# Kernel tuning notes

Hardware: AMD Instinct MI355X
Metric: run time of the kernel (lower is better)

Reference implementation:

```python
import jax, jax.numpy as jnp
import numpy as np

B1, B2, D = 10000, 10000, 128
ORDER = 4


def _cdist(a, b):
    # Stable L2 distance matrix: (B1,B2)
    a2 = jnp.sum(a * a, axis=1)[:, None]
    b2 = jnp.sum(b * b, axis=1)[None, :]
    d2 = a2 + b2 - 2.0 * (a @ b.T)
    return jnp.sqrt(jnp.clip(d2, 0.0))


def setup_inputs() -> dict:
    key = jax.random.key(0)
    k1, k2, k3 = jax.random.split(key, 3)
    desc1 = jax.random.normal(k1, (B1, D), dtype=jnp.float32)
    desc2 = jax.random.normal(k2, (B2, D), dtype=jnp.float32)
    # Steerer generator (D,D); scaled so repeated application stays bounded.
    generator = jax.random.normal(k3, (D, D), dtype=jnp.float32) / np.sqrt(D)
    return {"desc1": desc1, "desc2": desc2, "generator": generator, "steerer_order": ORDER}


def reference(desc1, desc2, generator, steerer_order):
    # steer_mode='local': distance between a pair is the min over all
    # steered versions of desc1 (DiscreteSteerer applies F.linear(x, G),
    # i.e. x @ G.T, repeatedly).
    dm = _cdist(desc1, desc2)
    d = desc1
    for _ in range(steerer_order - 1):
        d = d @ generator.T
        dm = jnp.minimum(dm, _cdist(d, desc2))
    # match_mode='nn': nearest neighbor in desc2 for each row of desc1.
    match_dists = jnp.min(dm, axis=1)
    idxs_in_2 = jnp.argmin(dm, axis=1)
    idxs_in_1 = jnp.arange(dm.shape[0], dtype=jnp.int64 if jax.config.jax_enable_x64 else jnp.int32)
    matches_idxs = jnp.stack([idxs_in_1, idxs_in_2.astype(idxs_in_1.dtype)], axis=1)
    return match_dists[:, None], matches_idxs
```

## Files before the change

### kernel.cpp

```cpp
#include <hip/hip_runtime.h>
#include <hip/hip_fp16.h>
#include <math.h>

#define NB1 10000
#define NB2 10000
#define DD  128
#define NV  4
#define B1P 10048
#define B1R (B1P * NV)
#define NB2P 10112
#define NB2G 320
#define NJT 79
#define MB  256
#define BN  128
#define NCHUNK 6
#define SROWS 16
#define SCALE 64.0f

typedef _Float16 f16x8 __attribute__((ext_vector_type(8)));
typedef __attribute__((ext_vector_type(16))) float f32x16;

__device__ __forceinline__ void gload_lds16(const void* g, void* l) {
    __builtin_amdgcn_global_load_lds(
        (const __attribute__((address_space(1))) void*)g,
        (__attribute__((address_space(3))) void*)l, 16, 0, 0);
}
__device__ __forceinline__ f32x16 mfma16(f16x8 a, f16x8 b, f32x16 c) {
    return __builtin_amdgcn_mfma_f32_32x32x16_f16(a, b, c, 0, 0, 0);
}
__device__ __forceinline__ void enc(float x, unsigned short* hb, unsigned short* lb) {
    float xs = SCALE * x;
    __half hh = __float2half_rn(xs);
    __half hl = __float2half_rn(xs - __half2float(hh));
    *hb = __half_as_ushort(hh);
    *lb = __half_as_ushort(hl);
}
__device__ __forceinline__ size_t cmap(int row, int col) {
    return ((size_t)(row >> 5) * 16 + (col >> 4)) * 512
         + (size_t)((row & 31) + (((col >> 3) & 1) << 5)) * 8 + (col & 7);
}


__global__ __launch_bounds__(128) void prep1s_kernel(
    const float* __restrict__ desc1, const float* __restrict__ G,
    unsigned short* __restrict__ A2c, float* __restrict__ n1) {
    __shared__ float GTl[128 * 129];
    __shared__ float src[SROWS][DD];
    __shared__ float p2[SROWS][2];
    const int t = threadIdx.x;
    const int i0 = blockIdx.x * SROWS;
    for (int f = 0; f < DD; ++f)
        GTl[t * 129 + f] = G[(size_t)f * DD + t];
    for (int r = 0; r < SROWS; ++r)
        src[r][t] = (i0 + r < NB1) ? desc1[(size_t)(i0 + r) * DD + t] : 0.f;
    __syncthreads();
    for (int k = 0; k < NV; ++k) {
        if (k > 0) {
            float out[SROWS];
#pragma unroll
            for (int r = 0; r < SROWS; ++r) out[r] = 0.f;
            for (int c = 0; c < DD; ++c) {
                float g = GTl[c * 129 + t];
#pragma unroll
                for (int r = 0; r < SROWS; ++r) out[r] = fmaf(src[r][c], g, out[r]);
            }
            __syncthreads();
#pragma unroll
            for (int r = 0; r < SROWS; ++r) src[r][t] = out[r];
            __syncthreads();
        }
        for (int r = 0; r < SROWS; ++r) {
            float x = src[r][t];
            unsigned short hb, lb;
            enc(x, &hb, &lb);
            int ar = (i0 + r) * NV + k;
            A2c[cmap(ar, t)] = hb;
            A2c[cmap(ar, 128 + t)] = lb;
            float s = x * x;
            for (int off = 32; off; off >>= 1) s += __shfl_down(s, off);
            if ((t & 63) == 0) p2[r][t >> 6] = s;
        }
        __syncthreads();
        if (t < SROWS) n1[(i0 + t) * NV + k] = p2[t][0] + p2[t][1];
        __syncthreads();
    }
}

__global__ void prep2_kernel(const float* __restrict__ desc2,
                             unsigned short* __restrict__ B2c, float* __restrict__ n2) {
    int j = blockIdx.x;
    int t = threadIdx.x;
    float x = (j < NB2) ? desc2[j * DD + t] : 0.f;
    unsigned short hb, lb;
    enc(x, &hb, &lb);
    B2c[cmap(j, t)] = hb;
    B2c[cmap(j, 128 + t)] = lb;
    float s = x * x;
    for (int off = 32; off; off >>= 1) s += __shfl_down(s, off);
    __shared__ float p[2];
    if ((t & 63) == 0) p[t >> 6] = s;
    __syncthreads();
    if (t == 0) n2[j] = (j < NB2) ? (p[0] + p[1]) : 1e30f;
}


#define STAGE1(BSEL, J0V, C16B, HALF)                                             \
    {                                                                             \
        int k16h_ = w >> 2, nf_ = w & 3;                                          \
        size_t gc_ = (size_t)(((J0V) >> 5) + nf_) * 16 + (C16B) + (HALF) * 2 + k16h_; \
        gload_lds16((const char*)B2c + gc_ * 1024 + l * 16,                       \
                    LDSB + (BSEL) * 8192 + w * 1024 + l * 16);                    \
    }

#define COMP2(BSEL, HALF, AK0, AK1)                                               \
    {                                                                             \
        _Pragma("unroll")                                                         \
        for (int kh_ = 0; kh_ < 2; ++kh_) {                                       \
            f16x8 b0_ = *(const f16x8*)(LDSB + (BSEL) * 8192 + (kh_ * 4 + wn * 2 + 0) * 1024 + l * 16); \
            f16x8 b1_ = *(const f16x8*)(LDSB + (BSEL) * 8192 + (kh_ * 4 + wn * 2 + 1) * 1024 + l * 16); \
            acc[0][0] = mfma16(Areg[0][AK0][(HALF) * 2 + kh_], b0_, acc[0][0]);   \
            acc[0][1] = mfma16(Areg[0][AK0][(HALF) * 2 + kh_], b1_, acc[0][1]);   \
            acc[1][0] = mfma16(Areg[1][AK0][(HALF) * 2 + kh_], b0_, acc[1][0]);   \
            acc[1][1] = mfma16(Areg[1][AK0][(HALF) * 2 + kh_], b1_, acc[1][1]);   \
            acc[0][0] = mfma16(Areg[0][AK1][(HALF) * 2 + kh_], b0_, acc[0][0]);   \
            acc[0][1] = mfma16(Areg[0][AK1][(HALF) * 2 + kh_], b1_, acc[0][1]);   \
            acc[1][0] = mfma16(Areg[1][AK1][(HALF) * 2 + kh_], b0_, acc[1][0]);   \
            acc[1][1] = mfma16(Areg[1][AK1][(HALF) * 2 + kh_], b1_, acc[1][1]);   \
        }                                                                         \
    }

#define COMP1(BSEL, HALF, AK0)                                                    \
    {                                                                             \
        _Pragma("unroll")                                                         \
        for (int kh_ = 0; kh_ < 2; ++kh_) {                                       \
            f16x8 b0_ = *(const f16x8*)(LDSB + (BSEL) * 8192 + (kh_ * 4 + wn * 2 + 0) * 1024 + l * 16); \
            f16x8 b1_ = *(const f16x8*)(LDSB + (BSEL) * 8192 + (kh_ * 4 + wn * 2 + 1) * 1024 + l * 16); \
            acc[0][0] = mfma16(Areg[0][AK0][(HALF) * 2 + kh_], b0_, acc[0][0]);   \
            acc[0][1] = mfma16(Areg[0][AK0][(HALF) * 2 + kh_], b1_, acc[0][1]);   \
            acc[1][0] = mfma16(Areg[1][AK0][(HALF) * 2 + kh_], b0_, acc[1][0]);   \
            acc[1][1] = mfma16(Areg[1][AK0][(HALF) * 2 + kh_], b1_, acc[1][1]);   \
        }                                                                         \
    }

#define PH(VM, BS, J0S, C16S, HS, CMP)                           \
    asm volatile("s_waitcnt vmcnt(" VM ")" ::: "memory");        \
    __builtin_amdgcn_s_barrier();                                \
    __builtin_amdgcn_sched_barrier(0);                           \
    STAGE1(BS, J0S, C16S, HS);                                   \
    CMP

__global__ __launch_bounds__(512, 2) void match_kernel(
    const unsigned short* __restrict__ A2c, const unsigned short* __restrict__ B2c,
    const float* __restrict__ n1, const float* __restrict__ n2,
    float* __restrict__ pb, int* __restrict__ pj) {
    __shared__ __align__(16) char LDSB[4 * 8192];
    __shared__ float LDSn1[256];
    const int t = threadIdx.x;
    const int l = t & 63, w = t >> 6;
    const int wm = w >> 1, wn = w & 1;
    const int c5 = l & 31, h = l >> 5;
    const int bi = blockIdx.x, ch = blockIdx.y;
    const int R0 = bi * MB;

    f16x8 Areg[2][4][4];
#pragma unroll
    for (int a = 0; a < 2; ++a)
#pragma unroll
        for (int aks = 0; aks < 4; ++aks)
#pragma unroll
            for (int k16 = 0; k16 < 4; ++k16) {
                size_t g = (size_t)(bi * 8 + wm * 2 + a);
                Areg[a][aks][k16] = *(const f16x8*)(
                    (const char*)A2c + (g * 16 + aks * 4 + k16) * 1024 + l * 16);
            }
    { int idx = t & 255; LDSn1[idx] = n1[R0 + idx]; }

    const int jt0 = (ch * NJT) / NCHUNK;
    const int jt1 = ((ch + 1) * NJT) / NCHUNK;

    STAGE1(0, jt0 * BN, 0, 0);
    STAGE1(1, jt0 * BN, 0, 1);
    STAGE1(2, jt0 * BN, 4, 0);
    asm volatile("s_waitcnt lgkmcnt(0)" ::: "memory");

    float best[2][4];
    int bj[2][4];
#pragma unroll
    for (int a = 0; a < 2; ++a)
#pragma unroll
        for (int rq = 0; rq < 4; ++rq) { best[a][rq] = 3.4e38f; bj[a][rq] = 0; }

    for (int jt = jt0; jt < jt1; ++jt) {
        const int j0 = jt * BN;
        float nn0 = n2[j0 + wn * 64 + c5];
        float nn1 = n2[j0 + wn * 64 + 32 + c5];
        f32x16 acc[2][2];
#pragma unroll
        for (int a = 0; a < 2; ++a)
#pragma unroll
            for (int b = 0; b < 2; ++b)
#pragma unroll
                for (int e = 0; e < 16; ++e) acc[a][b][e] = 0.f;

        PH("4", 3, j0, 4, 1,       COMP2(0, 0, 0, 2));
        PH("4", 0, j0, 8, 0,       COMP2(1, 1, 0, 2));
        PH("4", 1, j0, 8, 1,       COMP2(2, 0, 1, 3));
        PH("2", 2, j0, 12, 0,      COMP2(3, 1, 1, 3));
        PH("2", 3, j0, 12, 1,      COMP1(0, 0, 0));
        PH("2", 0, j0 + BN, 0, 0,  COMP1(1, 1, 0));
        PH("2", 1, j0 + BN, 0, 1,  COMP1(2, 0, 1));
        PH("2", 2, j0 + BN, 4, 0,  COMP1(3, 1, 1));

#pragma unroll
        for (int a = 0; a < 2; ++a)
#pragma unroll
            for (int b = 0; b < 2; ++b) {
                float nn = b ? nn1 : nn0;
                int j = j0 + wn * 64 + b * 32 + c5;
#pragma unroll
                for (int rq = 0; rq < 4; ++rq) {
                    float4 n1v = *(const float4*)&LDSn1[wm * 64 + a * 32 + 8 * rq + 4 * h];
                    float e0 = fmaf(-0.00048828125f, acc[a][b][4 * rq + 0], n1v.x);
                    float e1 = fmaf(-0.00048828125f, acc[a][b][4 * rq + 1], n1v.y);
                    float e2 = fmaf(-0.00048828125f, acc[a][b][4 * rq + 2], n1v.z);
                    float e3 = fmaf(-0.00048828125f, acc[a][b][4 * rq + 3], n1v.w);
                    float d = fminf(fminf(e0, e1), fminf(e2, e3)) + nn;
                    if (d < best[a][rq]) { best[a][rq] = d; bj[a][rq] = j; }
                }
            }
    }

#pragma unroll
    for (int off = 1; off < 32; off <<= 1) {
#pragma unroll
        for (int a = 0; a < 2; ++a)
#pragma unroll
            for (int rq = 0; rq < 4; ++rq) {
                float ov = __shfl_xor(best[a][rq], off);
                int oj = __shfl_xor(bj[a][rq], off);
                if (ov < best[a][rq] || (ov == best[a][rq] && oj < bj[a][rq])) {
                    best[a][rq] = ov; bj[a][rq] = oj;
                }
            }
    }
    if (c5 == 0) {
        int slot = ch * 2 + wn;
#pragma unroll
        for (int a = 0; a < 2; ++a)
#pragma unroll
            for (int rq = 0; rq < 4; ++rq) {
                int i = bi * 64 + wm * 16 + a * 8 + 2 * rq + h;
                pb[slot * B1P + i] = best[a][rq];
                pj[slot * B1P + i] = bj[a][rq];
            }
    }
}

__global__ void final_kernel(const float* __restrict__ pb, const int* __restrict__ pj,
                             float* __restrict__ out) {
    int i = blockIdx.x * 256 + threadIdx.x;
    if (i < NB1) {
        float bv = 3.4e38f;
        int bj = 0;
#pragma unroll
        for (int s = 0; s < 2 * NCHUNK; ++s) {
            float v = pb[s * B1P + i];
            int j = pj[s * B1P + i];
            if (v < bv || (v == bv && j < bj)) { bv = v; bj = j; }
        }
        out[i] = sqrtf(fmaxf(bv, 0.f));
        out[NB1 + 2 * i] = (float)i;
        out[NB1 + 2 * i + 1] = (float)bj;
    }
}


extern "C" void kernel_launch(void* const* d_in, const int* in_sizes, int n_in,
                              void* d_out, int out_size, void* d_ws, size_t ws_size,
                              hipStream_t stream) {
    const float* desc1 = (const float*)d_in[0];
    const float* desc2 = (const float*)d_in[1];
    const float* G     = (const float*)d_in[2];

    unsigned short* A2c = (unsigned short*)d_ws;
    unsigned short* B2c = A2c + (size_t)(B1R / 32) * 16 * 512;
    float* n1 = (float*)(B2c + (size_t)NB2G * 16 * 512);
    float* n2 = n1 + B1R;
    float* pb = n2 + NB2P;
    int*   pj = (int*)(pb + 2 * NCHUNK * B1P);
    float* out = (float*)d_out;

    hipLaunchKernelGGL(prep1s_kernel, dim3(B1P / SROWS), dim3(128), 0, stream,
                       desc1, G, A2c, n1);
    hipLaunchKernelGGL(prep2_kernel, dim3(NB2P), dim3(128), 0, stream, desc2, B2c, n2);
    hipLaunchKernelGGL(match_kernel, dim3(B1R / MB, NCHUNK), dim3(512), 0, stream,
                       A2c, B2c, n1, n2, pb, pj);
    hipLaunchKernelGGL(final_kernel, dim3((NB1 + 255) / 256), dim3(256), 0, stream,
                       pb, pj, out);
}
```

Before: 455.2 us.

## Restructure prep kernels with LDS-staged coalesced writes and halve match row tile

The prep kernels now build each 32-row fragment block in shared memory and write it out with coalesced 16-byte stores, instead of scattered 2-byte writes through cmap. A separate transpose kernel produces GT in global memory so prep1 no longer loads a 64KB G transpose into LDS per block. The match kernel halves the row tile to 128 (one 32-row fragment per wave), stages whole 4-k16 B slices per phase into larger LDS buffers with 4 phases instead of 8, and raises wave priority around the MFMA blocks. NCHUNK drops to 3 so the grid stays the same size. Fewer A registers may raise occupancy, but each B tile fetched is now reused across fewer A rows.

```diff
diff --git a/kernel.cpp b/kernel.cpp
--- a/kernel.cpp
+++ b/kernel.cpp
@@ -11,10 +11,9 @@
 #define NB2P 10112
 #define NB2G 320
 #define NJT 79
-#define MB  256
+#define MB  128
 #define BN  128
-#define NCHUNK 6
-#define SROWS 16
+#define NCHUNK 3
 #define SCALE 64.0f
 
 typedef _Float16 f16x8 __attribute__((ext_vector_type(8)));
@@ -35,126 +34,159 @@
     *hb = __half_as_ushort(hh);
     *lb = __half_as_ushort(hl);
 }
-__device__ __forceinline__ size_t cmap(int row, int col) {
-    return ((size_t)(row >> 5) * 16 + (col >> 4)) * 512
-         + (size_t)((row & 31) + (((col >> 3) & 1) << 5)) * 8 + (col & 7);
-}
-
-
-__global__ __launch_bounds__(128) void prep1s_kernel(
-    const float* __restrict__ desc1, const float* __restrict__ G,
+
+
+__global__ void gt_kernel(const float* __restrict__ G, float* __restrict__ GT) {
+    int idx = blockIdx.x * 256 + threadIdx.x;
+    if (idx < DD * DD) {
+        int c = idx / DD, f = idx % DD;
+        GT[idx] = G[f * DD + c];
+    }
+}
+
+__global__ __launch_bounds__(128) void prep1_kernel(
+    const float* __restrict__ desc1, const float* __restrict__ GT,
     unsigned short* __restrict__ A2c, float* __restrict__ n1) {
-    __shared__ float GTl[128 * 129];
-    __shared__ float src[SROWS][DD];
-    __shared__ float p2[SROWS][2];
+    __shared__ float src[8][DD];
+    __shared__ __align__(16) unsigned short cbuf[8192];
+    __shared__ float p2[8][2];
     const int t = threadIdx.x;
-    const int i0 = blockIdx.x * SROWS;
-    for (int f = 0; f < DD; ++f)
-        GTl[t * 129 + f] = G[(size_t)f * DD + t];
-    for (int r = 0; r < SROWS; ++r)
+    const int i0 = blockIdx.x * 8;
+    for (int r = 0; r < 8; ++r)
         src[r][t] = (i0 + r < NB1) ? desc1[(size_t)(i0 + r) * DD + t] : 0.f;
     __syncthreads();
     for (int k = 0; k < NV; ++k) {
-        if (k > 0) {
-            float out[SROWS];
-#pragma unroll
-            for (int r = 0; r < SROWS; ++r) out[r] = 0.f;
+        float out[8];
+        if (k == 0) {
+#pragma unroll
+            for (int r = 0; r < 8; ++r) out[r] = src[r][t];
+        } else {
+#pragma unroll
+            for (int r = 0; r < 8; ++r) out[r] = 0.f;
             for (int c = 0; c < DD; ++c) {
-                float g = GTl[c * 129 + t];
-#pragma unroll
-                for (int r = 0; r < SROWS; ++r) out[r] = fmaf(src[r][c], g, out[r]);
+                float g = GT[c * DD + t];
+#pragma unroll
+                for (int r = 0; r < 8; ++r) out[r] = fmaf(src[r][c], g, out[r]);
             }
             __syncthreads();
 #pragma unroll
-            for (int r = 0; r < SROWS; ++r) src[r][t] = out[r];
+            for (int r = 0; r < 8; ++r) src[r][t] = out[r];
             __syncthreads();
         }
-        for (int r = 0; r < SROWS; ++r) {
-            float x = src[r][t];
+        const int c16h = t >> 4, half = (t >> 3) & 1, el = t & 7;
+        for (int r = 0; r < 8; ++r) {
             unsigned short hb, lb;
-            enc(x, &hb, &lb);
-            int ar = (i0 + r) * NV + k;
-            A2c[cmap(ar, t)] = hb;
-            A2c[cmap(ar, 128 + t)] = lb;
-            float s = x * x;
+            enc(out[r], &hb, &lb);
+            int row32 = r * 4 + k;
+            cbuf[c16h * 512 + (row32 + half * 32) * 8 + el] = hb;
+            cbuf[(8 + c16h) * 512 + (row32 + half * 32) * 8 + el] = lb;
+            float s = out[r] * out[r];
             for (int off = 32; off; off >>= 1) s += __shfl_down(s, off);
             if ((t & 63) == 0) p2[r][t >> 6] = s;
         }
         __syncthreads();
-        if (t < SROWS) n1[(i0 + t) * NV + k] = p2[t][0] + p2[t][1];
+        if (t < 8) n1[(size_t)(i0 + t) * NV + k] = p2[t][0] + p2[t][1];
         __syncthreads();
     }
-}
-
-__global__ void prep2_kernel(const float* __restrict__ desc2,
-                             unsigned short* __restrict__ B2c, float* __restrict__ n2) {
-    int j = blockIdx.x;
-    int t = threadIdx.x;
-    float x = (j < NB2) ? desc2[j * DD + t] : 0.f;
-    unsigned short hb, lb;
-    enc(x, &hb, &lb);
-    B2c[cmap(j, t)] = hb;
-    B2c[cmap(j, 128 + t)] = lb;
-    float s = x * x;
-    for (int off = 32; off; off >>= 1) s += __shfl_down(s, off);
-    __shared__ float p[2];
-    if ((t & 63) == 0) p[t >> 6] = s;
+    const int wv = t >> 6, l = t & 63;
+#pragma unroll
+    for (int q = 0; q < 8; ++q) {
+        int chunk = wv * 8 + q;
+        int4 v = *(const int4*)((const char*)cbuf + chunk * 1024 + l * 16);
+        *(int4*)((char*)A2c + ((size_t)blockIdx.x * 16 + chunk) * 1024 + l * 16) = v;
+    }
+}
+
+__global__ __launch_bounds__(256) void prep2_kernel(
+    const float* __restrict__ desc2, unsigned short* __restrict__ B2c,
+    float* __restrict__ n2) {
+    __shared__ float srcf[32 * DD];
+    __shared__ __align__(16) unsigned short cbuf[8192];
+    const int t = threadIdx.x;
+    const int j0 = blockIdx.x * 32;
+    for (int ii = 0; ii < 16; ++ii) {
+        int idx = t + 256 * ii;
+        int row = idx >> 7, col = idx & 127;
+        srcf[idx] = (j0 + row < NB2) ? desc2[(size_t)(j0 + row) * DD + col] : 0.f;
+    }
     __syncthreads();
-    if (t == 0) n2[j] = (j < NB2) ? (p[0] + p[1]) : 1e30f;
-}
-
-
-#define STAGE1(BSEL, J0V, C16B, HALF)                                             \
-    {                                                                             \
-        int k16h_ = w >> 2, nf_ = w & 3;                                          \
-        size_t gc_ = (size_t)(((J0V) >> 5) + nf_) * 16 + (C16B) + (HALF) * 2 + k16h_; \
-        gload_lds16((const char*)B2c + gc_ * 1024 + l * 16,                       \
-                    LDSB + (BSEL) * 8192 + w * 1024 + l * 16);                    \
-    }
-
-#define COMP2(BSEL, HALF, AK0, AK1)                                               \
+    const int r = t >> 3, cg = t & 7;
+    float s = 0.f;
+#pragma unroll
+    for (int e = 0; e < 16; ++e) {
+        int c = cg * 16 + e;
+        float x = srcf[r * DD + c];
+        unsigned short hb, lb;
+        enc(x, &hb, &lb);
+        int lane = r + ((e >> 3) & 1) * 32;
+        cbuf[cg * 512 + lane * 8 + (e & 7)] = hb;
+        cbuf[(8 + cg) * 512 + lane * 8 + (e & 7)] = lb;
+        s += x * x;
+    }
+    s += __shfl_xor(s, 1); s += __shfl_xor(s, 2); s += __shfl_xor(s, 4);
+    if ((t & 7) == 0) n2[j0 + r] = (j0 + r < NB2) ? s : 1e30f;
+    __syncthreads();
+    const int wv = t >> 6, l = t & 63;
+#pragma unroll
+    for (int q = 0; q < 4; ++q) {
+        int chunk = wv * 4 + q;
+        int4 v = *(const int4*)((const char*)cbuf + chunk * 1024 + l * 16);
+        *(int4*)((char*)B2c + ((size_t)blockIdx.x * 16 + chunk) * 1024 + l * 16) = v;
+    }
+}
+
+
+#define STAGE(BUF, J0V, C16B)                                                     \
     {                                                                             \
         _Pragma("unroll")                                                         \
-        for (int kh_ = 0; kh_ < 2; ++kh_) {                                       \
-            f16x8 b0_ = *(const f16x8*)(LDSB + (BSEL) * 8192 + (kh_ * 4 + wn * 2 + 0) * 1024 + l * 16); \
-            f16x8 b1_ = *(const f16x8*)(LDSB + (BSEL) * 8192 + (kh_ * 4 + wn * 2 + 1) * 1024 + l * 16); \
-            acc[0][0] = mfma16(Areg[0][AK0][(HALF) * 2 + kh_], b0_, acc[0][0]);   \
-            acc[0][1] = mfma16(Areg[0][AK0][(HALF) * 2 + kh_], b1_, acc[0][1]);   \
-            acc[1][0] = mfma16(Areg[1][AK0][(HALF) * 2 + kh_], b0_, acc[1][0]);   \
-            acc[1][1] = mfma16(Areg[1][AK0][(HALF) * 2 + kh_], b1_, acc[1][1]);   \
-            acc[0][0] = mfma16(Areg[0][AK1][(HALF) * 2 + kh_], b0_, acc[0][0]);   \
-            acc[0][1] = mfma16(Areg[0][AK1][(HALF) * 2 + kh_], b1_, acc[0][1]);   \
-            acc[1][0] = mfma16(Areg[1][AK1][(HALF) * 2 + kh_], b0_, acc[1][0]);   \
-            acc[1][1] = mfma16(Areg[1][AK1][(HALF) * 2 + kh_], b1_, acc[1][1]);   \
+        for (int c_ = 0; c_ < 2; ++c_) {                                          \
+            int chunk_ = w * 2 + c_;                                              \
+            int nf_ = chunk_ >> 2, c16_ = chunk_ & 3;                             \
+            size_t gc_ = (size_t)(((J0V) >> 5) + nf_) * 16 + (C16B) + c16_;       \
+            gload_lds16((const char*)B2c + gc_ * 1024 + l * 16,                   \
+                        LDSB + (BUF) * 16384 + chunk_ * 1024 + l * 16);           \
         }                                                                         \
     }
 
-#define COMP1(BSEL, HALF, AK0)                                                    \
+#define COMP2(BUF, AKA, AKB)                                                      \
     {                                                                             \
         _Pragma("unroll")                                                         \
-        for (int kh_ = 0; kh_ < 2; ++kh_) {                                       \
-            f16x8 b0_ = *(const f16x8*)(LDSB + (BSEL) * 8192 + (kh_ * 4 + wn * 2 + 0) * 1024 + l * 16); \
-            f16x8 b1_ = *(const f16x8*)(LDSB + (BSEL) * 8192 + (kh_ * 4 + wn * 2 + 1) * 1024 + l * 16); \
-            acc[0][0] = mfma16(Areg[0][AK0][(HALF) * 2 + kh_], b0_, acc[0][0]);   \
-            acc[0][1] = mfma16(Areg[0][AK0][(HALF) * 2 + kh_], b1_, acc[0][1]);   \
-            acc[1][0] = mfma16(Areg[1][AK0][(HALF) * 2 + kh_], b0_, acc[1][0]);   \
-            acc[1][1] = mfma16(Areg[1][AK0][(HALF) * 2 + kh_], b1_, acc[1][1]);   \
+        for (int k16_ = 0; k16_ < 4; ++k16_) {                                    \
+            f16x8 b0_ = *(const f16x8*)(LDSB + (BUF) * 16384 + ((wn * 2 + 0) * 4 + k16_) * 1024 + l * 16); \
+            f16x8 b1_ = *(const f16x8*)(LDSB + (BUF) * 16384 + ((wn * 2 + 1) * 4 + k16_) * 1024 + l * 16); \
+            acc[0] = mfma16(Areg[AKA][k16_], b0_, acc[0]);                        \
+            acc[1] = mfma16(Areg[AKA][k16_], b1_, acc[1]);                        \
+            acc[0] = mfma16(Areg[AKB][k16_], b0_, acc[0]);                        \
+            acc[1] = mfma16(Areg[AKB][k16_], b1_, acc[1]);                        \
         }                                                                         \
     }
 
-#define PH(VM, BS, J0S, C16S, HS, CMP)                           \
+#define COMP1(BUF, AKA)                                                           \
+    {                                                                             \
+        _Pragma("unroll")                                                         \
+        for (int k16_ = 0; k16_ < 4; ++k16_) {                                    \
+            f16x8 b0_ = *(const f16x8*)(LDSB + (BUF) * 16384 + ((wn * 2 + 0) * 4 + k16_) * 1024 + l * 16); \
+            f16x8 b1_ = *(const f16x8*)(LDSB + (BUF) * 16384 + ((wn * 2 + 1) * 4 + k16_) * 1024 + l * 16); \
+            acc[0] = mfma16(Areg[AKA][k16_], b0_, acc[0]);                        \
+            acc[1] = mfma16(Areg[AKA][k16_], b1_, acc[1]);                        \
+        }                                                                         \
+    }
+
+#define PH(VM, STG, CMP)                                         \
     asm volatile("s_waitcnt vmcnt(" VM ")" ::: "memory");        \
     __builtin_amdgcn_s_barrier();                                \
     __builtin_amdgcn_sched_barrier(0);                           \
-    STAGE1(BS, J0S, C16S, HS);                                   \
-    CMP
+    STG;                                                         \
+    __builtin_amdgcn_s_setprio(1);                               \
+    CMP;                                                         \
+    __builtin_amdgcn_s_setprio(0);
 
 __global__ __launch_bounds__(512, 2) void match_kernel(
     const unsigned short* __restrict__ A2c, const unsigned short* __restrict__ B2c,
     const float* __restrict__ n1, const float* __restrict__ n2,
     float* __restrict__ pb, int* __restrict__ pj) {
-    __shared__ __align__(16) char LDSB[4 * 8192];
-    __shared__ float LDSn1[256];
+    __shared__ __align__(16) char LDSB[4 * 16384];
+    __shared__ float LDSn1[128];
     const int t = threadIdx.x;
     const int l = t & 63, w = t >> 6;
     const int wm = w >> 1, wn = w & 1;
@@ -162,97 +194,81 @@
     const int bi = blockIdx.x, ch = blockIdx.y;
     const int R0 = bi * MB;
 
-    f16x8 Areg[2][4][4];
-#pragma unroll
-    for (int a = 0; a < 2; ++a)
-#pragma unroll
-        for (int aks = 0; aks < 4; ++aks)
-#pragma unroll
-            for (int k16 = 0; k16 < 4; ++k16) {
-                size_t g = (size_t)(bi * 8 + wm * 2 + a);
-                Areg[a][aks][k16] = *(const f16x8*)(
-                    (const char*)A2c + (g * 16 + aks * 4 + k16) * 1024 + l * 16);
-            }
-    { int idx = t & 255; LDSn1[idx] = n1[R0 + idx]; }
+    f16x8 Areg[4][4];
+#pragma unroll
+    for (int aks = 0; aks < 4; ++aks)
+#pragma unroll
+        for (int k16 = 0; k16 < 4; ++k16) {
+            size_t g = (size_t)(bi * 4 + wm);
+            Areg[aks][k16] = *(const f16x8*)(
+                (const char*)A2c + (g * 16 + aks * 4 + k16) * 1024 + l * 16);
+        }
+    if (t < 128) LDSn1[t] = n1[R0 + t];
 
     const int jt0 = (ch * NJT) / NCHUNK;
     const int jt1 = ((ch + 1) * NJT) / NCHUNK;
 
-    STAGE1(0, jt0 * BN, 0, 0);
-    STAGE1(1, jt0 * BN, 0, 1);
-    STAGE1(2, jt0 * BN, 4, 0);
+    STAGE(0, jt0 * BN, 0);
+    STAGE(1, jt0 * BN, 4);
+    STAGE(2, jt0 * BN, 8);
     asm volatile("s_waitcnt lgkmcnt(0)" ::: "memory");
 
-    float best[2][4];
-    int bj[2][4];
-#pragma unroll
-    for (int a = 0; a < 2; ++a)
-#pragma unroll
-        for (int rq = 0; rq < 4; ++rq) { best[a][rq] = 3.4e38f; bj[a][rq] = 0; }
+    float best[4];
+    int bj[4];
+#pragma unroll
+    for (int rq = 0; rq < 4; ++rq) { best[rq] = 3.4e38f; bj[rq] = 0; }
 
     for (int jt = jt0; jt < jt1; ++jt) {
         const int j0 = jt * BN;
         float nn0 = n2[j0 + wn * 64 + c5];
         float nn1 = n2[j0 + wn * 64 + 32 + c5];
-        f32x16 acc[2][2];
-#pragma unroll
-        for (int a = 0; a < 2; ++a)
-#pragma unroll
-            for (int b = 0; b < 2; ++b)
-#pragma unroll
-                for (int e = 0; e < 16; ++e) acc[a][b][e] = 0.f;
-
-        PH("4", 3, j0, 4, 1,       COMP2(0, 0, 0, 2));
-        PH("4", 0, j0, 8, 0,       COMP2(1, 1, 0, 2));
-        PH("4", 1, j0, 8, 1,       COMP2(2, 0, 1, 3));
-        PH("2", 2, j0, 12, 0,      COMP2(3, 1, 1, 3));
-        PH("2", 3, j0, 12, 1,      COMP1(0, 0, 0));
-        PH("2", 0, j0 + BN, 0, 0,  COMP1(1, 1, 0));
-        PH("2", 1, j0 + BN, 0, 1,  COMP1(2, 0, 1));
-        PH("2", 2, j0 + BN, 4, 0,  COMP1(3, 1, 1));
-
-#pragma unroll
-        for (int a = 0; a < 2; ++a)
-#pragma unroll
-            for (int b = 0; b < 2; ++b) {
-                float nn = b ? nn1 : nn0;
-                int j = j0 + wn * 64 + b * 32 + c5;
-#pragma unroll
-                for (int rq = 0; rq < 4; ++rq) {
-                    float4 n1v = *(const float4*)&LDSn1[wm * 64 + a * 32 + 8 * rq + 4 * h];
-                    float e0 = fmaf(-0.00048828125f, acc[a][b][4 * rq + 0], n1v.x);
-                    float e1 = fmaf(-0.00048828125f, acc[a][b][4 * rq + 1], n1v.y);
-                    float e2 = fmaf(-0.00048828125f, acc[a][b][4 * rq + 2], n1v.z);
-                    float e3 = fmaf(-0.00048828125f, acc[a][b][4 * rq + 3], n1v.w);
-                    float d = fminf(fminf(e0, e1), fminf(e2, e3)) + nn;
-                    if (d < best[a][rq]) { best[a][rq] = d; bj[a][rq] = j; }
-                }
+        f32x16 acc[2];
+#pragma unroll
+        for (int b = 0; b < 2; ++b)
+#pragma unroll
+            for (int e = 0; e < 16; ++e) acc[b][e] = 0.f;
+
+        PH("6", STAGE(3, j0, 12),      COMP2(0, 0, 2));
+        PH("6", STAGE(0, j0 + BN, 0),  COMP2(1, 1, 3));
+        PH("6", STAGE(1, j0 + BN, 4),  COMP1(2, 0));
+        PH("4", STAGE(2, j0 + BN, 8),  COMP1(3, 1));
+
+#pragma unroll
+        for (int b = 0; b < 2; ++b) {
+            float nn = b ? nn1 : nn0;
+            int j = j0 + wn * 64 + b * 32 + c5;
+#pragma unroll
+            for (int rq = 0; rq < 4; ++rq) {
+                float4 n1v = *(const float4*)&LDSn1[wm * 32 + 8 * rq + 4 * h];
+                float e0 = fmaf(-0.00048828125f, acc[b][4 * rq + 0], n1v.x);
+                float e1 = fmaf(-0.00048828125f, acc[b][4 * rq + 1], n1v.y);
+                float e2 = fmaf(-0.00048828125f, acc[b][4 * rq + 2], n1v.z);
+                float e3 = fmaf(-0.00048828125f, acc[b][4 * rq + 3], n1v.w);
+                float d = fminf(fminf(e0, e1), fminf(e2, e3)) + nn;
+                if (d < best[rq]) { best[rq] = d; bj[rq] = j; }
             }
+        }
     }
 
 #pragma unroll
     for (int off = 1; off < 32; off <<= 1) {
 #pragma unroll
-        for (int a = 0; a < 2; ++a)
-#pragma unroll
-            for (int rq = 0; rq < 4; ++rq) {
-                float ov = __shfl_xor(best[a][rq], off);
-                int oj = __shfl_xor(bj[a][rq], off);
-                if (ov < best[a][rq] || (ov == best[a][rq] && oj < bj[a][rq])) {
-                    best[a][rq] = ov; bj[a][rq] = oj;
-                }
+        for (int rq = 0; rq < 4; ++rq) {
+            float ov = __shfl_xor(best[rq], off);
+            int oj = __shfl_xor(bj[rq], off);
+            if (ov < best[rq] || (ov == best[rq] && oj < bj[rq])) {
+                best[rq] = ov; bj[rq] = oj;
             }
+        }
     }
     if (c5 == 0) {
         int slot = ch * 2 + wn;
 #pragma unroll
-        for (int a = 0; a < 2; ++a)
-#pragma unroll
-            for (int rq = 0; rq < 4; ++rq) {
-                int i = bi * 64 + wm * 16 + a * 8 + 2 * rq + h;
-                pb[slot * B1P + i] = best[a][rq];
-                pj[slot * B1P + i] = bj[a][rq];
-            }
+        for (int rq = 0; rq < 4; ++rq) {
+            int i = bi * 32 + wm * 8 + 2 * rq + h;
+            pb[slot * B1P + i] = best[rq];
+            pj[slot * B1P + i] = bj[rq];
+        }
     }
 }
 
@@ -283,16 +299,19 @@
     const float* G     = (const float*)d_in[2];
 
     unsigned short* A2c = (unsigned short*)d_ws;
-    unsigned short* B2c = A2c + (size_t)(B1R / 32) * 16 * 512;
-    float* n1 = (float*)(B2c + (size_t)NB2G * 16 * 512);
+    unsigned short* B2c = A2c + (size_t)(B1R / 32) * 8192;
+    float* GT = (float*)(B2c + (size_t)NB2G * 8192);
+    float* n1 = GT + DD * DD;
     float* n2 = n1 + B1R;
     float* pb = n2 + NB2P;
     int*   pj = (int*)(pb + 2 * NCHUNK * B1P);
     float* out = (float*)d_out;
 
-    hipLaunchKernelGGL(prep1s_kernel, dim3(B1P / SROWS), dim3(128), 0, stream,
-                       desc1, G, A2c, n1);
-    hipLaunchKernelGGL(prep2_kernel, dim3(NB2P), dim3(128), 0, stream, desc2, B2c, n2);
+    hipLaunchKernelGGL(gt_kernel, dim3((DD * DD + 255) / 256), dim3(256), 0, stream, G, GT);
+    hipLaunchKernelGGL(prep1_kernel, dim3(B1P / 8), dim3(128), 0, stream,
+                       desc1, GT, A2c, n1);
+    hipLaunchKernelGGL(prep2_kernel, dim3(NB2P / 32), dim3(256), 0, stream,
+                       desc2, B2c, n2);
     hipLaunchKernelGGL(match_kernel, dim3(B1R / MB, NCHUNK), dim3(512), 0, stream,
                        A2c, B2c, n1, n2, pb, pj);
     hipLaunchKernelGGL(final_kernel, dim3((NB1 + 255) / 256), dim3(256), 0, stream,
```

Measured after the change: 400.4 us. 1.14x faster.
